# Performance work log

Measured on AMD Instinct MI355X. Metric: run time of the kernel, lower is better.

## Reference

```python
import jax, jax.numpy as jnp
import numpy as np

N_DRUG = 100000
N_PROT = 100000
N_EDGE = 800000
DIM = 128


def _graph_conv(feat_src, esrc, edst, n_src, n_dst, W, b):
    """dgl GraphConv with norm='both': msg = h_src * outdeg^-1/2, sum over in-edges,
    scale by indeg^-1/2, then linear. Degrees clamped to >= 1."""
    ones = jnp.ones(esrc.shape[0], dtype=feat_src.dtype)
    deg_out = jnp.clip(jax.ops.segment_sum(ones, esrc, num_segments=n_src), 1.0)
    deg_in = jnp.clip(jax.ops.segment_sum(ones, edst, num_segments=n_dst), 1.0)
    h = feat_src * jax.lax.rsqrt(deg_out)[:, None]          # [n_src, d]
    agg = jax.ops.segment_sum(h[esrc], edst, num_segments=n_dst)  # [n_dst, d]
    agg = agg * jax.lax.rsqrt(deg_in)[:, None]
    return agg @ W + b


def _hetero_layer(hd, hp, ddi_src, ddi_dst, pdi_src, pdi_dst, ppi_src, ppi_dst, W, b):
    # relation order: 0=DDI (drug->drug), 1=PDI (protein->drug), 2=PPI (protein->protein)
    d_ddi = _graph_conv(hd, ddi_src, ddi_dst, N_DRUG, N_DRUG, W[0], b[0])
    d_pdi = _graph_conv(hp, pdi_src, pdi_dst, N_PROT, N_DRUG, W[1], b[1])
    p_ppi = _graph_conv(hp, ppi_src, ppi_dst, N_PROT, N_PROT, W[2], b[2])
    return d_ddi + d_pdi, p_ppi  # HeteroGraphConv aggregate='sum' per dst type


def setup_inputs() -> dict:
    key = jax.random.key(0)
    ks = jax.random.split(key, 16)
    s = 1.0 / np.sqrt(DIM)
    return {
        "drug_feats": jax.random.normal(ks[0], (N_DRUG, DIM), jnp.float32),
        "protein_feats": jax.random.normal(ks[1], (N_PROT, DIM), jnp.float32),
        "ddi_src": jax.random.randint(ks[2], (N_EDGE,), 0, N_DRUG),
        "ddi_dst": jax.random.randint(ks[3], (N_EDGE,), 0, N_DRUG),
        "pdi_src": jax.random.randint(ks[4], (N_EDGE,), 0, N_PROT),
        "pdi_dst": jax.random.randint(ks[5], (N_EDGE,), 0, N_DRUG),
        "ppi_src": jax.random.randint(ks[6], (N_EDGE,), 0, N_PROT),
        "ppi_dst": jax.random.randint(ks[7], (N_EDGE,), 0, N_PROT),
        "W1": jax.random.normal(ks[8], (3, DIM, DIM), jnp.float32) * s,
        "b1": jnp.zeros((3, DIM), jnp.float32),
        "W2": jax.random.normal(ks[9], (3, DIM, DIM), jnp.float32) * s,
        "b2": jnp.zeros((3, DIM), jnp.float32),
        "W3": jax.random.normal(ks[10], (3, DIM, DIM), jnp.float32) * s,
        "b3": jnp.zeros((3, DIM), jnp.float32),
    }


def reference(drug_feats, protein_feats, ddi_src, ddi_dst, pdi_src, pdi_dst,
              ppi_src, ppi_dst, W1, b1, W2, b2, W3, b3):
    e = (ddi_src, ddi_dst, pdi_src, pdi_dst, ppi_src, ppi_dst)
    hd, hp = _hetero_layer(drug_feats, protein_feats, *e, W1, b1)
    hd, hp = jax.nn.relu(hd), jax.nn.relu(hp)
    hd, hp = _hetero_layer(hd, hp, *e, W2, b2)
    hd, hp = jax.nn.relu(hd), jax.nn.relu(hp)
    hd, hp = _hetero_layer(hd, hp, *e, W3, b3)
    return hd, hp
```

## Files before the change

### kernel.cpp

```cpp
#include <hip/hip_runtime.h>
#include <hip/hip_bf16.h>
#include <stdint.h>

#define NN 100000
#define NE 800000
#define SCAN_CHUNK 2048
#define NBLK 49

#define NPART 8
#define PART_SZ ((NN + NPART - 1) / NPART)
#define KSPLIT 16
#define SEGSZ (NE / KSPLIT)
#define HBINS PART_SZ

typedef __bf16 bf16x8 __attribute__((ext_vector_type(8)));
using float4v = __attribute__((ext_vector_type(4))) float;
typedef int intv4 __attribute__((ext_vector_type(4)));
typedef unsigned short ushortv4 __attribute__((ext_vector_type(4)));

__device__ __forceinline__ float bf2f(unsigned short h) {
    unsigned int u = ((unsigned int)h) << 16;
    return __builtin_bit_cast(float, u);
}
__device__ __forceinline__ float bf_lo(unsigned int u) {
    return __builtin_bit_cast(float, u << 16);
}
__device__ __forceinline__ float bf_hi(unsigned int u) {
    return __builtin_bit_cast(float, u & 0xffff0000u);
}
__device__ __forceinline__ unsigned short f2bf(float x) {
    unsigned int u = __builtin_bit_cast(unsigned int, x);
    u += 0x7fffu + ((u >> 16) & 1u);
    return (unsigned short)(u >> 16);
}

__global__ void detect_fmt(const unsigned short* __restrict__ feat, int* __restrict__ flag) {
    __shared__ int cnt;
    if (threadIdx.x == 0) cnt = 0;
    __syncthreads();
    unsigned int u = feat[threadIdx.x];
    int e = (u >> 7) & 0xFF;
    if (e >= 90 && e <= 143) atomicAdd(&cnt, 1);
    __syncthreads();
    if (threadIdx.x == 0) {
        flag[0] = (cnt >= 160) ? 0 : 1;
        flag[1] = 0;
    }
}

__global__ __launch_bounds__(256) void convert_feats(const void* __restrict__ drug,
                                                     const void* __restrict__ prot,
                                                     unsigned short* __restrict__ hd,
                                                     unsigned short* __restrict__ hp,
                                                     const int* __restrict__ fmtp) {
    int fmt = fmtp[0];
    int i = (blockIdx.x * 256 + threadIdx.x) * 4;
    const int n1 = NN * 128;
    if (i >= 2 * n1) return;
    const void* src = (i < n1) ? drug : prot;
    unsigned short* dst = (i < n1) ? hd : hp;
    int j = (i < n1) ? i : i - n1;
    if (fmt) {
        float4 v = *(const float4*)((const float*)src + j);
        uint2 o;
        o.x = (unsigned int)f2bf(v.x) | ((unsigned int)f2bf(v.y) << 16);
        o.y = (unsigned int)f2bf(v.z) | ((unsigned int)f2bf(v.w) << 16);
        *(uint2*)(dst + j) = o;
    } else {
        *(uint2*)(dst + j) = *(const uint2*)((const unsigned short*)src + j);
    }
}

__global__ __launch_bounds__(256) void deg_hist(const int* __restrict__ s0, const int* __restrict__ d0,
                                                const int* __restrict__ s1, const int* __restrict__ d1,
                                                const int* __restrict__ s2, const int* __restrict__ d2,
                                                unsigned short* __restrict__ deg_part) {
    __shared__ unsigned int cnt[HBINS];
    int h = blockIdx.y;
    const int* a;
    switch (h) {
        case 0: a = s0; break;
        case 1: a = s1; break;
        case 2: a = s2; break;
        case 3: a = d0; break;
        case 4: a = d1; break;
        default: a = d2; break;
    }
    int part = blockIdx.x & (NPART - 1);
    int seg = blockIdx.x >> 3;
    int lo = part * HBINS;
    for (int j = threadIdx.x; j < HBINS; j += 256) cnt[j] = 0;
    __syncthreads();
    int base = seg * SEGSZ;
    int end = base + SEGSZ;
    for (int i = base + threadIdx.x * 4; i + 4 <= end; i += 1024) {
        intv4 v = *(const intv4*)(a + i);
#pragma unroll
        for (int k = 0; k < 4; k++) {
            int b = v[k] - lo;
            if ((unsigned)b < (unsigned)HBINS) atomicAdd(&cnt[b], 1u);
        }
    }
    __syncthreads();
    unsigned short* outp = deg_part + (size_t)seg * 6 * NN + (size_t)h * NN + lo;
    for (int j = threadIdx.x; j < HBINS; j += 256) outp[j] = (unsigned short)cnt[j];
}

__global__ __launch_bounds__(256) void merge_deg_rs(const unsigned short* __restrict__ deg_part,
                                                    int* __restrict__ deg_all,
                                                    float* __restrict__ rs_all) {
    int i = (blockIdx.x * 256 + threadIdx.x) * 4;
    if (i >= 6 * NN) return;
    int a0 = 0, a1 = 0, a2 = 0, a3 = 0;
#pragma unroll
    for (int s = 0; s < KSPLIT; s++) {
        ushortv4 v = *(const ushortv4*)(deg_part + (size_t)s * 6 * NN + i);
        a0 += v[0]; a1 += v[1]; a2 += v[2]; a3 += v[3];
    }
    intv4 acc; acc[0] = a0; acc[1] = a1; acc[2] = a2; acc[3] = a3;
    *(intv4*)(deg_all + i) = acc;
    float4v r;
#pragma unroll
    for (int k = 0; k < 4; k++) {
        int d = acc[k];
        if (d < 1) d = 1;
        r[k] = rsqrtf((float)d);
    }
    *(float4v*)(rs_all + i) = r;
}

__global__ __launch_bounds__(256) void scan_partial(const int* __restrict__ deg,
                                                    int* __restrict__ bsums) {
    int rel = blockIdx.y, blk = blockIdx.x;
    const int* d = deg + rel * NN;
    int base = blk * SCAN_CHUNK + threadIdx.x * 8;
    int s = 0;
#pragma unroll
    for (int i = 0; i < 8; i++) {
        int idx = base + i;
        if (idx < NN) s += d[idx];
    }
    __shared__ int wsum[4];
#pragma unroll
    for (int off = 32; off; off >>= 1) s += __shfl_down(s, off);
    if ((threadIdx.x & 63) == 0) wsum[threadIdx.x >> 6] = s;
    __syncthreads();
    if (threadIdx.x == 0) bsums[rel * NBLK + blk] = wsum[0] + wsum[1] + wsum[2] + wsum[3];
}

__global__ void scan_bsums(int* bsums) {
    int r = threadIdx.x;
    if (r < 3) {
        int run = 0;
        for (int i = 0; i < NBLK; i++) {
            int t = bsums[r * NBLK + i];
            bsums[r * NBLK + i] = run;
            run += t;
        }
    }
}

__global__ __launch_bounds__(256) void scan_final(const int* __restrict__ deg,
                                                  const int* __restrict__ bsums,
                                                  int* __restrict__ offs) {
    int rel = blockIdx.y, blk = blockIdx.x;
    const int* d = deg + rel * NN;
    int* o = offs + rel * NN;
    int base = blk * SCAN_CHUNK + threadIdx.x * 8;
    int v[8];
    int s = 0;
#pragma unroll
    for (int i = 0; i < 8; i++) {
        int idx = base + i;
        v[i] = (idx < NN) ? d[idx] : 0;
        s += v[i];
    }
    int lane = threadIdx.x & 63, wid = threadIdx.x >> 6;
    int x = s;
#pragma unroll
    for (int off = 1; off < 64; off <<= 1) {
        int t = __shfl_up(x, off);
        if (lane >= off) x += t;
    }
    __shared__ int wsum[4];
    if (lane == 63) wsum[wid] = x;
    __syncthreads();
    int woff = bsums[rel * NBLK + blk];
    for (int i = 0; i < wid; i++) woff += wsum[i];
    int run = woff + x - s;
#pragma unroll
    for (int i = 0; i < 8; i++) {
        int idx = base + i;
        if (idx < NN) {
            o[idx] = run;
            run += v[i];
        }
    }
}

__global__ __launch_bounds__(256) void seg_start_k(const unsigned short* __restrict__ deg_part,
                                                   const int* __restrict__ offs_all,
                                                   int* __restrict__ seg_start) {
    int i = blockIdx.x * 256 + threadIdx.x;
    if (i >= 3 * NN) return;
    int rel = i / NN, node = i - rel * NN;
    int run = offs_all[i];
#pragma unroll
    for (int s = 0; s < KSPLIT; s++) {
        seg_start[((size_t)s * 3 + rel) * NN + node] = run;
        run += deg_part[((size_t)s * 6 + 3 + rel) * NN + node];
    }
}

__global__ __launch_bounds__(256) void csr_fill3s(const int* __restrict__ s0, const int* __restrict__ d0,
                                                  const int* __restrict__ s1, const int* __restrict__ d1,
                                                  const int* __restrict__ s2, const int* __restrict__ d2,
                                                  const int* __restrict__ seg_start,
                                                  int* __restrict__ csr_all) {
    __shared__ int cur[PART_SZ];
    int rel = blockIdx.y;
    const int* s = (rel == 0) ? s0 : ((rel == 1) ? s1 : s2);
    const int* d = (rel == 0) ? d0 : ((rel == 1) ? d1 : d2);
    int part = blockIdx.x & (NPART - 1);
    int seg = blockIdx.x >> 3;
    int lo = part * PART_SZ;
    const int* ss = seg_start + ((size_t)seg * 3 + rel) * NN + lo;
    for (int j = threadIdx.x; j < PART_SZ; j += 256) cur[j] = ss[j];
    __syncthreads();
    int* csr = csr_all + (size_t)rel * NE;
    int base = seg * SEGSZ;
    int end = base + SEGSZ;
    for (int i = base + threadIdx.x * 4; i + 4 <= end; i += 1024) {
        intv4 dv = *(const intv4*)(d + i);
        intv4 sv = *(const intv4*)(s + i);
#pragma unroll
        for (int k = 0; k < 4; k++) {
            int b = dv[k] - lo;
            if ((unsigned)b < (unsigned)PART_SZ) {
                int pos = atomicAdd(&cur[b], 1);
                csr[pos] = sv[k];
            }
        }
    }
}

__global__ __launch_bounds__(256) void swizzle_w3(const void* __restrict__ W0,
                                                  const void* __restrict__ W1,
                                                  const void* __restrict__ W2,
                                                  int o0, int o1,
                                                  unsigned short* __restrict__ out, int lstride,
                                                  const int* __restrict__ fmtp, int ksteps) {
    int l = blockIdx.y;
    const void* W = (l == 0) ? W0 : ((l == 1) ? W1 : W2);
    int fmt = fmtp[0];
    int idx = blockIdx.x * 256 + threadIdx.x;
    int total = ksteps * 8 * 64 * 8;
    if (idx >= total) return;
    int j = idx & 7, lane = (idx >> 3) & 63, nt = (idx >> 9) & 7, ks = idx >> 12;
    int k = ks * 32 + (lane >> 4) * 8 + j;
    int n = nt * 16 + (lane & 15);
    int e = (k < 128) ? (o0 + k * 128 + n) : (o1 + (k - 128) * 128 + n);
    out[l * lstride + idx] = fmt ? f2bf(((const float*)W)[e]) : ((const unsigned short*)W)[e];
}

__global__ void bias_prep3(const void* __restrict__ b0, const void* __restrict__ b1,
                           const void* __restrict__ b2, float* __restrict__ bd,
                           float* __restrict__ bp, const int* __restrict__ fmtp) {
    int l = blockIdx.x;
    const void* b = (l == 0) ? b0 : ((l == 1) ? b1 : b2);
    int fmt = fmtp[0];
    int n = threadIdx.x;
    float v0, v1, v2;
    if (fmt) {
        const float* bf = (const float*)b;
        v0 = bf[n]; v1 = bf[128 + n]; v2 = bf[256 + n];
    } else {
        const unsigned short* bh = (const unsigned short*)b;
        v0 = bf2f(bh[n]); v1 = bf2f(bh[128 + n]); v2 = bf2f(bh[256 + n]);
    }
    bd[l * 128 + n] = v0 + v1;
    bp[l * 128 + n] = v2;
}

__device__ __forceinline__ void acc8(float* acc, uint4 v, float w) {
    acc[0] = fmaf(bf_lo(v.x), w, acc[0]);
    acc[1] = fmaf(bf_hi(v.x), w, acc[1]);
    acc[2] = fmaf(bf_lo(v.y), w, acc[2]);
    acc[3] = fmaf(bf_hi(v.y), w, acc[3]);
    acc[4] = fmaf(bf_lo(v.z), w, acc[4]);
    acc[5] = fmaf(bf_hi(v.z), w, acc[5]);
    acc[6] = fmaf(bf_lo(v.w), w, acc[6]);
    acc[7] = fmaf(bf_hi(v.w), w, acc[7]);
}

__global__ __launch_bounds__(256) void agg_gemm(const unsigned short* __restrict__ hd,
                                                const unsigned short* __restrict__ hp,
                                                const float* __restrict__ rs_all,
                                                const int* __restrict__ offs_all,
                                                const int* __restrict__ deg_in_all,
                                                const int* __restrict__ csr_all,
                                                const unsigned short* __restrict__ Wd,
                                                const unsigned short* __restrict__ Wp,
                                                const float* __restrict__ bdl,
                                                const float* __restrict__ bpl,
                                                void* __restrict__ outD, size_t obD,
                                                void* __restrict__ outP, size_t obP,
                                                int relu, const int* __restrict__ ofmt) {
    __shared__ unsigned short as[64][264];
    int y = blockIdx.y;
    int tid = threadIdx.x;
    int grp = tid >> 4, lane = tid & 15;
    int base = blockIdx.x * 64;

    int nrel = y ? 1 : 2;
    for (int rr = 0; rr < nrel; rr++) {
        int rel = y ? 2 : rr;
        const unsigned short* h = (rel == 0) ? hd : hp;
        const float* rs_out = rs_all + rel * NN;
        const float* rs_in = rs_all + (3 + rel) * NN;
        int ocol = (rr == 1) ? 128 : 0;
#pragma unroll
        for (int i = 0; i < 4; i++) {
            int dl = grp * 4 + i;
            int dst = base + dl;
            if (dst > NN - 1) dst = NN - 1;
            const int* cp = csr_all + (size_t)rel * NE + offs_all[rel * NN + dst];
            int cnt = deg_in_all[rel * NN + dst];
            float acc[8] = {0.f, 0.f, 0.f, 0.f, 0.f, 0.f, 0.f, 0.f};
            int e = 0;
            for (; e + 4 <= cnt; e += 4) {
                int i0 = cp[e], i1 = cp[e + 1], i2 = cp[e + 2], i3 = cp[e + 3];
                float w0 = rs_out[i0], w1 = rs_out[i1], w2 = rs_out[i2], w3 = rs_out[i3];
                uint4 v0 = *(const uint4*)(h + (size_t)i0 * 128 + lane * 8);
                uint4 v1 = *(const uint4*)(h + (size_t)i1 * 128 + lane * 8);
                uint4 v2 = *(const uint4*)(h + (size_t)i2 * 128 + lane * 8);
                uint4 v3 = *(const uint4*)(h + (size_t)i3 * 128 + lane * 8);
                acc8(acc, v0, w0);
                acc8(acc, v1, w1);
                acc8(acc, v2, w2);
                acc8(acc, v3, w3);
            }
            for (; e < cnt; e++) {
                int i0 = cp[e];
                float w0 = rs_out[i0];
                uint4 v0 = *(const uint4*)(h + (size_t)i0 * 128 + lane * 8);
                acc8(acc, v0, w0);
            }
            float sc = rs_in[dst];
            uint4 o;
            o.x = (unsigned int)f2bf(acc[0] * sc) | ((unsigned int)f2bf(acc[1] * sc) << 16);
            o.y = (unsigned int)f2bf(acc[2] * sc) | ((unsigned int)f2bf(acc[3] * sc) << 16);
            o.z = (unsigned int)f2bf(acc[4] * sc) | ((unsigned int)f2bf(acc[5] * sc) << 16);
            o.w = (unsigned int)f2bf(acc[6] * sc) | ((unsigned int)f2bf(acc[7] * sc) << 16);
            *(uint4*)(&as[dl][ocol + lane * 8]) = o;
        }
    }
    __syncthreads();

    const unsigned short* Bf = y ? Wp : Wd;
    const float* bias = y ? bpl : bdl;
    void* outv = y ? outP : outD;
    size_t obase = y ? obP : obD;
    int nch = y ? 1 : 2;
    int fmt = ofmt[0];
    int lid = tid & 63, wid = tid >> 6;
    int ar = wid * 16 + (lid & 15);
    int koff = (lid >> 4) * 8;
    float4v acc[8];
#pragma unroll
    for (int nt = 0; nt < 8; nt++) acc[nt] = (float4v){0.f, 0.f, 0.f, 0.f};
    for (int c = 0; c < nch; c++) {
#pragma unroll
        for (int ks = 0; ks < 4; ks++) {
            bf16x8 a = *(const bf16x8*)(&as[ar][c * 128 + ks * 32 + koff]);
            const bf16x8* bp8 = (const bf16x8*)(Bf + (size_t)c * 16384) + ks * 8 * 64 + lid;
#pragma unroll
            for (int nt = 0; nt < 8; nt++) {
                bf16x8 b = bp8[nt * 64];
                acc[nt] = __builtin_amdgcn_mfma_f32_16x16x32_bf16(a, b, acc[nt], 0, 0, 0);
            }
        }
    }
    int crow = base + wid * 16 + (lid >> 4) * 4;
    int ccol = lid & 15;
#pragma unroll
    for (int nt = 0; nt < 8; nt++) {
        float bb = bias[nt * 16 + ccol];
#pragma unroll
        for (int r = 0; r < 4; r++) {
            int row = crow + r;
            if (row < NN) {
                float yv = acc[nt][r] + bb;
                if (relu) yv = fmaxf(yv, 0.f);
                size_t idx = obase + (size_t)row * 128 + nt * 16 + ccol;
                if (fmt) ((float*)outv)[idx] = yv;
                else ((unsigned short*)outv)[idx] = f2bf(yv);
            }
        }
    }
}

extern "C" void kernel_launch(void* const* d_in, const int* in_sizes, int n_in,
                              void* d_out, int out_size, void* d_ws, size_t ws_size,
                              hipStream_t stream) {
    (void)in_sizes; (void)n_in; (void)out_size;
    const void* drug = d_in[0];
    const void* prot = d_in[1];
    const int* ddi_src = (const int*)d_in[2];
    const int* ddi_dst = (const int*)d_in[3];
    const int* pdi_src = (const int*)d_in[4];
    const int* pdi_dst = (const int*)d_in[5];
    const int* ppi_src = (const int*)d_in[6];
    const int* ppi_dst = (const int*)d_in[7];
    const void* Wl[3] = {d_in[8], d_in[10], d_in[12]};
    const void* bl[3] = {d_in[9], d_in[11], d_in[13]};

    char* p = (char*)d_ws;
    auto alloc = [&](size_t bytes) -> char* {
        char* r = p;
        p += (bytes + 255) & ~(size_t)255;
        return r;
    };
    int*   flag       = (int*)alloc(256);
    int*   deg_all    = (int*)alloc(6 * NN * 4);
    float* rs_all     = (float*)alloc(6 * NN * 4);
    int*   offs_all   = (int*)alloc(3 * NN * 4);
    int*   csr_all    = (int*)alloc(3 * NE * 4);
    int*   bsums      = (int*)alloc(3 * NBLK * 4);
    int*   seg_start  = (int*)alloc((size_t)KSPLIT * 3 * NN * 4);
    char*  hbuf       = alloc((size_t)NN * 128 * 4);
    unsigned short* hd_b = (unsigned short*)hbuf;
    unsigned short* hp_b = (unsigned short*)hbuf + (size_t)NN * 128;
    unsigned short* Wd_f = (unsigned short*)alloc(3 * 8 * 8 * 64 * 8 * 2);
    unsigned short* Wp_f = (unsigned short*)alloc(3 * 4 * 8 * 64 * 8 * 2);
    float* bd = (float*)alloc(3 * 128 * 4);
    float* bp = (float*)alloc(3 * 128 * 4);
    size_t needed = (size_t)(p - (char*)d_ws);
    if (needed > ws_size) return;

    unsigned short* deg_part = (unsigned short*)hbuf;

    const int* FMT = flag;
    const int* BF  = flag + 1;

    unsigned short* hd_o = (unsigned short*)d_out;
    unsigned short* hp_o = (unsigned short*)d_out + (size_t)NN * 128;

    detect_fmt<<<1, 256, 0, stream>>>((const unsigned short*)drug, flag);

    deg_hist<<<dim3(NPART * KSPLIT, 6), 256, 0, stream>>>(ddi_src, ddi_dst, pdi_src, pdi_dst,
                                                          ppi_src, ppi_dst, deg_part);
    merge_deg_rs<<<(6 * NN / 4 + 255) / 256, 256, 0, stream>>>(deg_part, deg_all, rs_all);
    scan_partial<<<dim3(NBLK, 3), 256, 0, stream>>>(deg_all + 3 * NN, bsums);
    scan_bsums<<<1, 64, 0, stream>>>(bsums);
    scan_final<<<dim3(NBLK, 3), 256, 0, stream>>>(deg_all + 3 * NN, bsums, offs_all);
    seg_start_k<<<(3 * NN + 255) / 256, 256, 0, stream>>>(deg_part, offs_all, seg_start);
    csr_fill3s<<<dim3(NPART * KSPLIT, 3), 256, 0, stream>>>(ddi_src, ddi_dst, pdi_src, pdi_dst,
                                                            ppi_src, ppi_dst, seg_start, csr_all);

    swizzle_w3<<<dim3((8 * 8 * 64 * 8 + 255) / 256, 3), 256, 0, stream>>>(
        Wl[0], Wl[1], Wl[2], 0, 16384, Wd_f, 32768, FMT, 8);
    swizzle_w3<<<dim3((4 * 8 * 64 * 8 + 255) / 256, 3), 256, 0, stream>>>(
        Wl[0], Wl[1], Wl[2], 32768, 0, Wp_f, 16384, FMT, 4);
    bias_prep3<<<3, 128, 0, stream>>>(bl[0], bl[1], bl[2], bd, bp, FMT);

    convert_feats<<<(2 * NN * 128 / 4 + 255) / 256, 256, 0, stream>>>(drug, prot, hd_b, hp_b, FMT);

    const int GGB = (NN + 63) / 64;
    agg_gemm<<<dim3(GGB, 2), 256, 0, stream>>>(hd_b, hp_b, rs_all, offs_all, deg_all + 3 * NN,
                                               csr_all, Wd_f, Wp_f, bd, bp,
                                               d_out, 0, d_out, (size_t)NN * 128, 1, BF);
    agg_gemm<<<dim3(GGB, 2), 256, 0, stream>>>(hd_o, hp_o, rs_all, offs_all, deg_all + 3 * NN,
                                               csr_all, Wd_f + 32768, Wp_f + 16384,
                                               bd + 128, bp + 128,
                                               hbuf, 0, hbuf, (size_t)NN * 128, 1, BF);
    agg_gemm<<<dim3(GGB, 2), 256, 0, stream>>>(hd_b, hp_b, rs_all, offs_all, deg_all + 3 * NN,
                                               csr_all, Wd_f + 2 * 32768, Wp_f + 2 * 16384,
                                               bd + 2 * 128, bp + 2 * 128,
                                               d_out, 0, d_out, (size_t)NN * 128, 0, FMT);
}
```

Baseline: 752.2 us.

## Transform-then-aggregate: apply GEMM before gather, split into separate GEMM and gather kernels

Reorders each graph conv so the linear projection runs first on node features (gemmT), then a separate gather kernel sums the projected rows with degree normalisation, bias and ReLU. This removes the LDS staging and fused GEMM from the gather kernel, drops the separate feature-conversion pass, and lets the gather run with one 16-lane group per destination node. It also doubles KSPLIT and packs two 16-bit histogram counters per shared word. The risks are an extra round trip of projected features through memory, aliasing of the transformed buffers with workspace (seg_start reused as Tws) and in-place GEMM writes to the same buffer it reads, plus an added bf16 rounding of the projected features before aggregation.

After: 697.0 us. -7.3%, faster.

```diff
diff --git a/kernel.cpp b/kernel.cpp
--- a/kernel.cpp
+++ b/kernel.cpp
@@ -9,7 +9,7 @@
 
 #define NPART 8
 #define PART_SZ ((NN + NPART - 1) / NPART)
-#define KSPLIT 16
+#define KSPLIT 32
 #define SEGSZ (NE / KSPLIT)
 #define HBINS PART_SZ
 
@@ -48,34 +48,11 @@
     }
 }
 
-__global__ __launch_bounds__(256) void convert_feats(const void* __restrict__ drug,
-                                                     const void* __restrict__ prot,
-                                                     unsigned short* __restrict__ hd,
-                                                     unsigned short* __restrict__ hp,
-                                                     const int* __restrict__ fmtp) {
-    int fmt = fmtp[0];
-    int i = (blockIdx.x * 256 + threadIdx.x) * 4;
-    const int n1 = NN * 128;
-    if (i >= 2 * n1) return;
-    const void* src = (i < n1) ? drug : prot;
-    unsigned short* dst = (i < n1) ? hd : hp;
-    int j = (i < n1) ? i : i - n1;
-    if (fmt) {
-        float4 v = *(const float4*)((const float*)src + j);
-        uint2 o;
-        o.x = (unsigned int)f2bf(v.x) | ((unsigned int)f2bf(v.y) << 16);
-        o.y = (unsigned int)f2bf(v.z) | ((unsigned int)f2bf(v.w) << 16);
-        *(uint2*)(dst + j) = o;
-    } else {
-        *(uint2*)(dst + j) = *(const uint2*)((const unsigned short*)src + j);
-    }
-}
-
 __global__ __launch_bounds__(256) void deg_hist(const int* __restrict__ s0, const int* __restrict__ d0,
                                                 const int* __restrict__ s1, const int* __restrict__ d1,
                                                 const int* __restrict__ s2, const int* __restrict__ d2,
                                                 unsigned short* __restrict__ deg_part) {
-    __shared__ unsigned int cnt[HBINS];
+    __shared__ unsigned int cnt[HBINS / 2];
     int h = blockIdx.y;
     const int* a;
     switch (h) {
@@ -89,7 +66,7 @@
     int part = blockIdx.x & (NPART - 1);
     int seg = blockIdx.x >> 3;
     int lo = part * HBINS;
-    for (int j = threadIdx.x; j < HBINS; j += 256) cnt[j] = 0;
+    for (int j = threadIdx.x; j < HBINS / 2; j += 256) cnt[j] = 0;
     __syncthreads();
     int base = seg * SEGSZ;
     int end = base + SEGSZ;
@@ -98,12 +75,12 @@
 #pragma unroll
         for (int k = 0; k < 4; k++) {
             int b = v[k] - lo;
-            if ((unsigned)b < (unsigned)HBINS) atomicAdd(&cnt[b], 1u);
-        }
-    }
-    __syncthreads();
-    unsigned short* outp = deg_part + (size_t)seg * 6 * NN + (size_t)h * NN + lo;
-    for (int j = threadIdx.x; j < HBINS; j += 256) outp[j] = (unsigned short)cnt[j];
+            if ((unsigned)b < (unsigned)HBINS) atomicAdd(&cnt[b >> 1], 1u << ((b & 1) * 16));
+        }
+    }
+    __syncthreads();
+    unsigned int* outp = (unsigned int*)(deg_part + (size_t)seg * 6 * NN + (size_t)h * NN + lo);
+    for (int j = threadIdx.x; j < HBINS / 2; j += 256) outp[j] = cnt[j];
 }
 
 __global__ __launch_bounds__(256) void merge_deg_rs(const unsigned short* __restrict__ deg_part,
@@ -244,23 +221,22 @@
     }
 }
 
-__global__ __launch_bounds__(256) void swizzle_w3(const void* __restrict__ W0,
+__global__ __launch_bounds__(256) void swizzle_w9(const void* __restrict__ W0,
                                                   const void* __restrict__ W1,
                                                   const void* __restrict__ W2,
-                                                  int o0, int o1,
-                                                  unsigned short* __restrict__ out, int lstride,
-                                                  const int* __restrict__ fmtp, int ksteps) {
-    int l = blockIdx.y;
+                                                  unsigned short* __restrict__ Wf,
+                                                  const int* __restrict__ fmtp) {
+    int yy = blockIdx.y;
+    int l = yy / 3, rel = yy - l * 3;
     const void* W = (l == 0) ? W0 : ((l == 1) ? W1 : W2);
     int fmt = fmtp[0];
     int idx = blockIdx.x * 256 + threadIdx.x;
-    int total = ksteps * 8 * 64 * 8;
-    if (idx >= total) return;
+    if (idx >= 16384) return;
     int j = idx & 7, lane = (idx >> 3) & 63, nt = (idx >> 9) & 7, ks = idx >> 12;
     int k = ks * 32 + (lane >> 4) * 8 + j;
     int n = nt * 16 + (lane & 15);
-    int e = (k < 128) ? (o0 + k * 128 + n) : (o1 + (k - 128) * 128 + n);
-    out[l * lstride + idx] = fmt ? f2bf(((const float*)W)[e]) : ((const unsigned short*)W)[e];
+    int e = rel * 16384 + k * 128 + n;
+    Wf[(size_t)yy * 16384 + idx] = fmt ? f2bf(((const float*)W)[e]) : ((const unsigned short*)W)[e];
 }
 
 __global__ void bias_prep3(const void* __restrict__ b0, const void* __restrict__ b1,
@@ -282,7 +258,68 @@
     bp[l * 128 + n] = v2;
 }
 
-__device__ __forceinline__ void acc8(float* acc, uint4 v, float w) {
+__global__ __launch_bounds__(256) void gemmT(const void* __restrict__ Ad,
+                                             const void* __restrict__ Ap,
+                                             const unsigned short* __restrict__ Wf,
+                                             unsigned short* __restrict__ T0,
+                                             unsigned short* __restrict__ T1,
+                                             unsigned short* __restrict__ T2,
+                                             const int* __restrict__ ifmtp) {
+    int y = blockIdx.y;
+    int ifmt = ifmtp[0];
+    const void* A = y ? Ap : Ad;
+    int lid = threadIdx.x & 63, wid = threadIdx.x >> 6;
+    int m0 = blockIdx.x * 64 + wid * 16;
+    int ra = m0 + (lid & 15);
+    if (ra > NN - 1) ra = NN - 1;
+    int koff = (lid >> 4) * 8;
+    bf16x8 a[4];
+    if (ifmt) {
+        const float* Af = (const float*)A + (size_t)ra * 128 + koff;
+#pragma unroll
+        for (int ks = 0; ks < 4; ks++) {
+            float4 u = *(const float4*)(Af + ks * 32);
+            float4 v = *(const float4*)(Af + ks * 32 + 4);
+            union { bf16x8 b; unsigned short s[8]; } t;
+            t.s[0] = f2bf(u.x); t.s[1] = f2bf(u.y); t.s[2] = f2bf(u.z); t.s[3] = f2bf(u.w);
+            t.s[4] = f2bf(v.x); t.s[5] = f2bf(v.y); t.s[6] = f2bf(v.z); t.s[7] = f2bf(v.w);
+            a[ks] = t.b;
+        }
+    } else {
+        const unsigned short* Ah = (const unsigned short*)A + (size_t)ra * 128 + koff;
+#pragma unroll
+        for (int ks = 0; ks < 4; ks++) a[ks] = *(const bf16x8*)(Ah + ks * 32);
+    }
+    int nouts = y ? 2 : 1;
+    for (int o = 0; o < nouts; o++) {
+        int rel = y ? (1 + o) : 0;
+        const bf16x8* bb = (const bf16x8*)(Wf + (size_t)rel * 16384);
+        float4v acc[8];
+#pragma unroll
+        for (int nt = 0; nt < 8; nt++) acc[nt] = (float4v){0.f, 0.f, 0.f, 0.f};
+#pragma unroll
+        for (int ks = 0; ks < 4; ks++) {
+#pragma unroll
+            for (int nt = 0; nt < 8; nt++) {
+                bf16x8 b = bb[ks * 512 + nt * 64 + lid];
+                acc[nt] = __builtin_amdgcn_mfma_f32_16x16x32_bf16(a[ks], b, acc[nt], 0, 0, 0);
+            }
+        }
+        unsigned short* T = (rel == 0) ? T0 : ((rel == 1) ? T1 : T2);
+        int crow = m0 + (lid >> 4) * 4;
+        int ccol = lid & 15;
+#pragma unroll
+        for (int nt = 0; nt < 8; nt++) {
+#pragma unroll
+            for (int r = 0; r < 4; r++) {
+                int row = crow + r;
+                if (row < NN) T[(size_t)row * 128 + nt * 16 + ccol] = f2bf(acc[nt][r]);
+            }
+        }
+    }
+}
+
+__device__ __forceinline__ void acc8v(float* acc, uint4 v, float w) {
     acc[0] = fmaf(bf_lo(v.x), w, acc[0]);
     acc[1] = fmaf(bf_hi(v.x), w, acc[1]);
     acc[2] = fmaf(bf_lo(v.y), w, acc[2]);
@@ -293,110 +330,104 @@
     acc[7] = fmaf(bf_hi(v.w), w, acc[7]);
 }
 
-__global__ __launch_bounds__(256) void agg_gemm(const unsigned short* __restrict__ hd,
-                                                const unsigned short* __restrict__ hp,
-                                                const float* __restrict__ rs_all,
-                                                const int* __restrict__ offs_all,
-                                                const int* __restrict__ deg_in_all,
-                                                const int* __restrict__ csr_all,
-                                                const unsigned short* __restrict__ Wd,
-                                                const unsigned short* __restrict__ Wp,
-                                                const float* __restrict__ bdl,
-                                                const float* __restrict__ bpl,
-                                                void* __restrict__ outD, size_t obD,
-                                                void* __restrict__ outP, size_t obP,
-                                                int relu, const int* __restrict__ ofmt) {
-    __shared__ unsigned short as[64][264];
+__device__ __forceinline__ void gather8(const unsigned short* __restrict__ T,
+                                        const float* __restrict__ rs_out,
+                                        const int* __restrict__ cp, int cnt, int lane,
+                                        float* acc) {
+    int e = 0;
+    for (; e + 4 <= cnt; e += 4) {
+        int i0 = cp[e], i1 = cp[e + 1], i2 = cp[e + 2], i3 = cp[e + 3];
+        float w0 = rs_out[i0], w1 = rs_out[i1], w2 = rs_out[i2], w3 = rs_out[i3];
+        uint4 v0 = *(const uint4*)(T + (size_t)i0 * 128 + lane * 8);
+        uint4 v1 = *(const uint4*)(T + (size_t)i1 * 128 + lane * 8);
+        uint4 v2 = *(const uint4*)(T + (size_t)i2 * 128 + lane * 8);
+        uint4 v3 = *(const uint4*)(T + (size_t)i3 * 128 + lane * 8);
+        acc8v(acc, v0, w0);
+        acc8v(acc, v1, w1);
+        acc8v(acc, v2, w2);
+        acc8v(acc, v3, w3);
+    }
+    for (; e < cnt; e++) {
+        int i0 = cp[e];
+        float w0 = rs_out[i0];
+        uint4 v0 = *(const uint4*)(T + (size_t)i0 * 128 + lane * 8);
+        acc8v(acc, v0, w0);
+    }
+}
+
+__global__ __launch_bounds__(256) void agg_out(const unsigned short* __restrict__ T0,
+                                               const unsigned short* __restrict__ T1,
+                                               const unsigned short* __restrict__ T2,
+                                               const float* __restrict__ rs_all,
+                                               const int* __restrict__ offs_all,
+                                               const int* __restrict__ deg_in_all,
+                                               const int* __restrict__ csr_all,
+                                               const float* __restrict__ bdl,
+                                               const float* __restrict__ bpl,
+                                               void* __restrict__ outv,
+                                               int relu, const int* __restrict__ ofmt) {
     int y = blockIdx.y;
-    int tid = threadIdx.x;
-    int grp = tid >> 4, lane = tid & 15;
-    int base = blockIdx.x * 64;
-
-    int nrel = y ? 1 : 2;
-    for (int rr = 0; rr < nrel; rr++) {
-        int rel = y ? 2 : rr;
-        const unsigned short* h = (rel == 0) ? hd : hp;
-        const float* rs_out = rs_all + rel * NN;
-        const float* rs_in = rs_all + (3 + rel) * NN;
-        int ocol = (rr == 1) ? 128 : 0;
-#pragma unroll
-        for (int i = 0; i < 4; i++) {
-            int dl = grp * 4 + i;
-            int dst = base + dl;
-            if (dst > NN - 1) dst = NN - 1;
-            const int* cp = csr_all + (size_t)rel * NE + offs_all[rel * NN + dst];
-            int cnt = deg_in_all[rel * NN + dst];
+    int g = blockIdx.x * 256 + threadIdx.x;
+    int dst = g >> 4;
+    int lane = g & 15;
+    if (dst >= NN) return;
+    int fmt = ofmt[0];
+    float out8[8] = {0.f, 0.f, 0.f, 0.f, 0.f, 0.f, 0.f, 0.f};
+    const float* bias;
+    int row;
+    if (y == 0) {
+        {
+            const int* cp = csr_all + offs_all[dst];
+            int cnt = deg_in_all[dst];
             float acc[8] = {0.f, 0.f, 0.f, 0.f, 0.f, 0.f, 0.f, 0.f};
-            int e = 0;
-            for (; e + 4 <= cnt; e += 4) {
-                int i0 = cp[e], i1 = cp[e + 1], i2 = cp[e + 2], i3 = cp[e + 3];
-                float w0 = rs_out[i0], w1 = rs_out[i1], w2 = rs_out[i2], w3 = rs_out[i3];
-                uint4 v0 = *(const uint4*)(h + (size_t)i0 * 128 + lane * 8);
-                uint4 v1 = *(const uint4*)(h + (size_t)i1 * 128 + lane * 8);
-                uint4 v2 = *(const uint4*)(h + (size_t)i2 * 128 + lane * 8);
-                uint4 v3 = *(const uint4*)(h + (size_t)i3 * 128 + lane * 8);
-                acc8(acc, v0, w0);
-                acc8(acc, v1, w1);
-                acc8(acc, v2, w2);
-                acc8(acc, v3, w3);
-            }
-            for (; e < cnt; e++) {
-                int i0 = cp[e];
-                float w0 = rs_out[i0];
-                uint4 v0 = *(const uint4*)(h + (size_t)i0 * 128 + lane * 8);
-                acc8(acc, v0, w0);
-            }
-            float sc = rs_in[dst];
-            uint4 o;
-            o.x = (unsigned int)f2bf(acc[0] * sc) | ((unsigned int)f2bf(acc[1] * sc) << 16);
-            o.y = (unsigned int)f2bf(acc[2] * sc) | ((unsigned int)f2bf(acc[3] * sc) << 16);
-            o.z = (unsigned int)f2bf(acc[4] * sc) | ((unsigned int)f2bf(acc[5] * sc) << 16);
-            o.w = (unsigned int)f2bf(acc[6] * sc) | ((unsigned int)f2bf(acc[7] * sc) << 16);
-            *(uint4*)(&as[dl][ocol + lane * 8]) = o;
-        }
-    }
-    __syncthreads();
-
-    const unsigned short* Bf = y ? Wp : Wd;
-    const float* bias = y ? bpl : bdl;
-    void* outv = y ? outP : outD;
-    size_t obase = y ? obP : obD;
-    int nch = y ? 1 : 2;
-    int fmt = ofmt[0];
-    int lid = tid & 63, wid = tid >> 6;
-    int ar = wid * 16 + (lid & 15);
-    int koff = (lid >> 4) * 8;
-    float4v acc[8];
-#pragma unroll
-    for (int nt = 0; nt < 8; nt++) acc[nt] = (float4v){0.f, 0.f, 0.f, 0.f};
-    for (int c = 0; c < nch; c++) {
-#pragma unroll
-        for (int ks = 0; ks < 4; ks++) {
-            bf16x8 a = *(const bf16x8*)(&as[ar][c * 128 + ks * 32 + koff]);
-            const bf16x8* bp8 = (const bf16x8*)(Bf + (size_t)c * 16384) + ks * 8 * 64 + lid;
-#pragma unroll
-            for (int nt = 0; nt < 8; nt++) {
-                bf16x8 b = bp8[nt * 64];
-                acc[nt] = __builtin_amdgcn_mfma_f32_16x16x32_bf16(a, b, acc[nt], 0, 0, 0);
-            }
-        }
-    }
-    int crow = base + wid * 16 + (lid >> 4) * 4;
-    int ccol = lid & 15;
-#pragma unroll
-    for (int nt = 0; nt < 8; nt++) {
-        float bb = bias[nt * 16 + ccol];
-#pragma unroll
-        for (int r = 0; r < 4; r++) {
-            int row = crow + r;
-            if (row < NN) {
-                float yv = acc[nt][r] + bb;
-                if (relu) yv = fmaxf(yv, 0.f);
-                size_t idx = obase + (size_t)row * 128 + nt * 16 + ccol;
-                if (fmt) ((float*)outv)[idx] = yv;
-                else ((unsigned short*)outv)[idx] = f2bf(yv);
-            }
-        }
+            gather8(T0, rs_all, cp, cnt, lane, acc);
+            float si = rs_all[3 * NN + dst];
+#pragma unroll
+            for (int j = 0; j < 8; j++) out8[j] = fmaf(si, acc[j], out8[j]);
+        }
+        {
+            const int* cp = csr_all + NE + offs_all[NN + dst];
+            int cnt = deg_in_all[NN + dst];
+            float acc[8] = {0.f, 0.f, 0.f, 0.f, 0.f, 0.f, 0.f, 0.f};
+            gather8(T1, rs_all + NN, cp, cnt, lane, acc);
+            float si = rs_all[4 * NN + dst];
+#pragma unroll
+            for (int j = 0; j < 8; j++) out8[j] = fmaf(si, acc[j], out8[j]);
+        }
+        bias = bdl;
+        row = dst;
+    } else {
+        const int* cp = csr_all + 2 * NE + offs_all[2 * NN + dst];
+        int cnt = deg_in_all[2 * NN + dst];
+        float acc[8] = {0.f, 0.f, 0.f, 0.f, 0.f, 0.f, 0.f, 0.f};
+        gather8(T2, rs_all + 2 * NN, cp, cnt, lane, acc);
+        float si = rs_all[5 * NN + dst];
+#pragma unroll
+        for (int j = 0; j < 8; j++) out8[j] = si * acc[j];
+        bias = bpl;
+        row = NN + dst;
+    }
+    float v[8];
+#pragma unroll
+    for (int j = 0; j < 8; j++) {
+        float t = out8[j] + bias[lane * 8 + j];
+        v[j] = relu ? fmaxf(t, 0.f) : t;
+    }
+    size_t base = (size_t)row * 128 + lane * 8;
+    if (fmt) {
+        float* o = (float*)outv + base;
+        float4 u0; u0.x = v[0]; u0.y = v[1]; u0.z = v[2]; u0.w = v[3];
+        float4 u1; u1.x = v[4]; u1.y = v[5]; u1.z = v[6]; u1.w = v[7];
+        *(float4*)o = u0;
+        *(float4*)(o + 4) = u1;
+    } else {
+        unsigned short* o = (unsigned short*)outv + base;
+        uint4 u;
+        u.x = (unsigned int)f2bf(v[0]) | ((unsigned int)f2bf(v[1]) << 16);
+        u.y = (unsigned int)f2bf(v[2]) | ((unsigned int)f2bf(v[3]) << 16);
+        u.z = (unsigned int)f2bf(v[4]) | ((unsigned int)f2bf(v[5]) << 16);
+        u.w = (unsigned int)f2bf(v[6]) | ((unsigned int)f2bf(v[7]) << 16);
+        *(uint4*)o = u;
     }
 }
 
@@ -429,22 +460,22 @@
     int*   bsums      = (int*)alloc(3 * NBLK * 4);
     int*   seg_start  = (int*)alloc((size_t)KSPLIT * 3 * NN * 4);
     char*  hbuf       = alloc((size_t)NN * 128 * 4);
-    unsigned short* hd_b = (unsigned short*)hbuf;
-    unsigned short* hp_b = (unsigned short*)hbuf + (size_t)NN * 128;
-    unsigned short* Wd_f = (unsigned short*)alloc(3 * 8 * 8 * 64 * 8 * 2);
-    unsigned short* Wp_f = (unsigned short*)alloc(3 * 4 * 8 * 64 * 8 * 2);
+    unsigned short* hbuf_lo = (unsigned short*)hbuf;
+    unsigned short* hbuf_hi = (unsigned short*)hbuf + (size_t)NN * 128;
+    unsigned short* Wf = (unsigned short*)alloc(9 * 16384 * 2);
     float* bd = (float*)alloc(3 * 128 * 4);
     float* bp = (float*)alloc(3 * 128 * 4);
     size_t needed = (size_t)(p - (char*)d_ws);
     if (needed > ws_size) return;
 
     unsigned short* deg_part = (unsigned short*)hbuf;
+    unsigned short* Tws = (unsigned short*)seg_start;
 
     const int* FMT = flag;
     const int* BF  = flag + 1;
 
-    unsigned short* hd_o = (unsigned short*)d_out;
-    unsigned short* hp_o = (unsigned short*)d_out + (size_t)NN * 128;
+    unsigned short* dout_lo = (unsigned short*)d_out;
+    unsigned short* dout_hi = (unsigned short*)d_out + (size_t)NN * 128;
 
     detect_fmt<<<1, 256, 0, stream>>>((const unsigned short*)drug, flag);
 
@@ -458,24 +489,23 @@
     csr_fill3s<<<dim3(NPART * KSPLIT, 3), 256, 0, stream>>>(ddi_src, ddi_dst, pdi_src, pdi_dst,
                                                             ppi_src, ppi_dst, seg_start, csr_all);
 
-    swizzle_w3<<<dim3((8 * 8 * 64 * 8 + 255) / 256, 3), 256, 0, stream>>>(
-        Wl[0], Wl[1], Wl[2], 0, 16384, Wd_f, 32768, FMT, 8);
-    swizzle_w3<<<dim3((4 * 8 * 64 * 8 + 255) / 256, 3), 256, 0, stream>>>(
-        Wl[0], Wl[1], Wl[2], 32768, 0, Wp_f, 16384, FMT, 4);
+    swizzle_w9<<<dim3(64, 9), 256, 0, stream>>>(Wl[0], Wl[1], Wl[2], Wf, FMT);
     bias_prep3<<<3, 128, 0, stream>>>(bl[0], bl[1], bl[2], bd, bp, FMT);
 
-    convert_feats<<<(2 * NN * 128 / 4 + 255) / 256, 256, 0, stream>>>(drug, prot, hd_b, hp_b, FMT);
-
-    const int GGB = (NN + 63) / 64;
-    agg_gemm<<<dim3(GGB, 2), 256, 0, stream>>>(hd_b, hp_b, rs_all, offs_all, deg_all + 3 * NN,
-                                               csr_all, Wd_f, Wp_f, bd, bp,
-                                               d_out, 0, d_out, (size_t)NN * 128, 1, BF);
-    agg_gemm<<<dim3(GGB, 2), 256, 0, stream>>>(hd_o, hp_o, rs_all, offs_all, deg_all + 3 * NN,
-                                               csr_all, Wd_f + 32768, Wp_f + 16384,
-                                               bd + 128, bp + 128,
-                                               hbuf, 0, hbuf, (size_t)NN * 128, 1, BF);
-    agg_gemm<<<dim3(GGB, 2), 256, 0, stream>>>(hd_b, hp_b, rs_all, offs_all, deg_all + 3 * NN,
-                                               csr_all, Wd_f + 2 * 32768, Wp_f + 2 * 16384,
-                                               bd + 2 * 128, bp + 2 * 128,
-                                               d_out, 0, d_out, (size_t)NN * 128, 0, FMT);
-}
+    const int TGB = (NN + 63) / 64;
+    const int AGB = (NN * 16) / 256;
+    gemmT<<<dim3(TGB, 2), 256, 0, stream>>>(drug, prot, Wf, hbuf_lo, hbuf_hi, Tws, FMT);
+    agg_out<<<dim3(AGB, 2), 256, 0, stream>>>(hbuf_lo, hbuf_hi, Tws, rs_all, offs_all,
+                                              deg_all + 3 * NN, csr_all, bd, bp,
+                                              d_out, 1, BF);
+    gemmT<<<dim3(TGB, 2), 256, 0, stream>>>(dout_lo, dout_hi, Wf + 3 * 16384,
+                                            dout_lo, dout_hi, Tws, BF);
+    agg_out<<<dim3(AGB, 2), 256, 0, stream>>>(dout_lo, dout_hi, Tws, rs_all, offs_all,
+                                              deg_all + 3 * NN, csr_all, bd + 128, bp + 128,
+                                              hbuf, 1, BF);
+    gemmT<<<dim3(TGB, 2), 256, 0, stream>>>(hbuf_lo, hbuf_hi, Wf + 6 * 16384,
+                                            hbuf_lo, hbuf_hi, Tws, BF);
+    agg_out<<<dim3(AGB, 2), 256, 0, stream>>>(hbuf_lo, hbuf_hi, Tws, rs_all, offs_all,
+                                              deg_all + 3 * NN, csr_all, bd + 2 * 128, bp + 2 * 128,
+                                              d_out, 0, FMT);
+}
```
